# Kernel tuning notes

Hardware: AMD Instinct MI355X
Metric: run time of the kernel (lower is better)

## Reference

```python
import jax, jax.numpy as jnp
import numpy as np

B, LQ, LKV, D = 16, 2048, 2048, 64
MASK_VALUE = -1000000.0


def setup_inputs() -> dict:
    key = jax.random.key(0)
    kq, kk, kv, kl = jax.random.split(key, 4)
    queries = jax.random.normal(kq, (B, LQ, D), dtype=jnp.float32)
    keys = jax.random.normal(kk, (B, LKV, D), dtype=jnp.float32)
    values = jax.random.normal(kv, (B, LKV, D), dtype=jnp.float32)
    valid_lens = jax.random.randint(kl, (B,), 1, LKV + 1, dtype=jnp.int32)
    return {"queries": queries, "keys": keys, "values": values, "valid_lens": valid_lens}


def reference(queries, keys, values, valid_lens):
    d = queries.shape[-1]
    # scores: [B, Lq, Lkv]
    scores = jnp.einsum('bqd,bkd->bqk', queries, keys) / jnp.sqrt(jnp.float32(d))
    # valid_lens is per-batch; positions >= valid_len are masked to -1e6 (not -inf),
    # matching torch masked_fill semantics before softmax.
    col = jnp.arange(scores.shape[-1], dtype=jnp.int32)            # [Lkv]
    mask = col[None, None, :] >= valid_lens[:, None, None]          # [B, 1, Lkv] -> broadcast over Lq
    scores = jnp.where(mask, jnp.float32(MASK_VALUE), scores)
    attn = jax.nn.softmax(scores, axis=-1)
    # dropout p=0.0 (eval) -> identity
    return jnp.einsum('bqk,bkd->bqd', attn, values)
```

## Files before the change

kernel.cpp:

```cpp
#include <hip/hip_runtime.h>
#include <hip/hip_bf16.h>


#define NB   16
#define LQS  2048
#define LKVS 2048
#define DH   64
#define QBLK 64
#define KVB  64

typedef short bf16x8 __attribute__((ext_vector_type(8)));
typedef float f32x4  __attribute__((ext_vector_type(4)));

__device__ __forceinline__ unsigned short f2bf(float x) {
    return __builtin_bit_cast(unsigned short, __float2bfloat16(x));
}
__device__ __forceinline__ float bf2f(unsigned short h) {
    return __uint_as_float(((unsigned int)h) << 16);
}

__global__ __launch_bounds__(512, 4) void attn_fa(
    const float* __restrict__ Qg, const float* __restrict__ Kg,
    const float* __restrict__ Vg, const int* __restrict__ vlg,
    float* __restrict__ Og)
{
    __shared__ __align__(16) unsigned short sMem[2][4 * KVB * DH];

    const int b    = blockIdx.y;
    const int q0   = blockIdx.x * QBLK;
    const int tid  = threadIdx.x;
    const int wg   = tid >> 8;
    const int gtid = tid & 255;
    const int w4   = (tid >> 6) & 3;
    const int lane = tid & 63;
    const int lr   = lane & 15;
    const int lg   = lane >> 4;
    const int n_valid = vlg[b];

    unsigned short* sKhi = &sMem[wg][0];
    unsigned short* sKlo = &sMem[wg][4096];
    unsigned short* sVhi = &sMem[wg][8192];
    unsigned short* sVlo = &sMem[wg][12288];

    bf16x8 qhi[2], qlo[2];
    {
        const float* qp = Qg + ((size_t)b * LQS + q0 + w4 * 16 + lr) * DH;
        #pragma unroll
        for (int s = 0; s < 2; ++s) {
            const float4 a = *(const float4*)(qp + s * 32 + lg * 8);
            const float4 c = *(const float4*)(qp + s * 32 + lg * 8 + 4);
            const float vv[8] = {a.x, a.y, a.z, a.w, c.x, c.y, c.z, c.w};
            #pragma unroll
            for (int i = 0; i < 8; ++i) {
                const float x = vv[i] * 0.125f;
                const unsigned short h = f2bf(x);
                qhi[s][i] = (short)h;
                qlo[s][i] = (short)f2bf(x - bf2f(h));
            }
        }
    }

    f32x4 o[4];
    #pragma unroll
    for (int nt = 0; nt < 4; ++nt) { o[nt][0]=0.f; o[nt][1]=0.f; o[nt][2]=0.f; o[nt][3]=0.f; }
    float m_q = -__builtin_inff();
    float l_q = 0.f;

    const int nsteps = (n_valid + KVB - 1) / KVB;
    const int rounds = (nsteps + 1) >> 1;
    for (int jt = 0; jt < rounds; ++jt) {
        const int st  = 2 * jt + wg;
        const bool act = (st < nsteps);
        const int kv0 = st * KVB;
        __syncthreads();
        if (act) {
            const float* kp = Kg + ((size_t)b * LKVS + kv0) * DH;
            const float* vp = Vg + ((size_t)b * LKVS + kv0) * DH;
            #pragma unroll
            for (int it = 0; it < 4; ++it) {
                const int idx = gtid + it * 256;
                const int key = idx >> 4, f4 = idx & 15;
                const float4 kq = *(const float4*)(kp + key * DH + f4 * 4);
                const float ka[4] = {kq.x, kq.y, kq.z, kq.w};
                unsigned short kh[4], kl[4];
                #pragma unroll
                for (int i = 0; i < 4; ++i) {
                    kh[i] = f2bf(ka[i]);
                    kl[i] = f2bf(ka[i] - bf2f(kh[i]));
                }
                const int kb_ = key * 64 + (((f4 * 4) & ~7) ^ ((key & 7) << 3)) + (f4 & 1) * 4;
                *(ushort4*)(&sKhi[kb_]) = make_ushort4(kh[0], kh[1], kh[2], kh[3]);
                *(ushort4*)(&sKlo[kb_]) = make_ushort4(kl[0], kl[1], kl[2], kl[3]);
            }
            {
                const int kb = (gtid >> 4) * 4;
                const int db = (gtid & 15) * 4;
                const int pb = (kb & ~31) | (((kb >> 2) & 3) << 3) | (((kb >> 4) & 1) << 2);
                const float4 vr0 = *(const float4*)(vp + (kb + 0) * DH + db);
                const float4 vr1 = *(const float4*)(vp + (kb + 1) * DH + db);
                const float4 vr2 = *(const float4*)(vp + (kb + 2) * DH + db);
                const float4 vr3 = *(const float4*)(vp + (kb + 3) * DH + db);
                #pragma unroll
                for (int i = 0; i < 4; ++i) {
                    const int d = db + i;
                    const float f0 = (&vr0.x)[i], f1 = (&vr1.x)[i];
                    const float f2_ = (&vr2.x)[i], f3 = (&vr3.x)[i];
                    const unsigned short h0 = f2bf(f0), h1 = f2bf(f1);
                    const unsigned short h2 = f2bf(f2_), h3 = f2bf(f3);
                    const int vi = d * 64 + (pb ^ ((d & 7) << 3));
                    *(ushort4*)(&sVhi[vi]) = make_ushort4(h0, h1, h2, h3);
                    *(ushort4*)(&sVlo[vi]) = make_ushort4(
                        f2bf(f0 - bf2f(h0)), f2bf(f1 - bf2f(h1)),
                        f2bf(f2_ - bf2f(h2)), f2bf(f3 - bf2f(h3)));
                }
            }
        }
        __syncthreads();
        if (act) {
            float p_[4][4];
            __builtin_amdgcn_s_setprio(1);
            #pragma unroll
            for (int kt = 0; kt < 4; ++kt) {
                f32x4 acc = {0.f, 0.f, 0.f, 0.f};
                const int key = kt * 16 + lr;
                #pragma unroll
                for (int s = 0; s < 2; ++s) {
                    const int ki = key * 64 + ((s * 32 + lg * 8) ^ ((key & 7) << 3));
                    const bf16x8 khi = *(const bf16x8*)(&sKhi[ki]);
                    const bf16x8 klo = *(const bf16x8*)(&sKlo[ki]);
                    acc = __builtin_amdgcn_mfma_f32_16x16x32_bf16(khi, qhi[s], acc, 0, 0, 0);
                    acc = __builtin_amdgcn_mfma_f32_16x16x32_bf16(khi, qlo[s], acc, 0, 0, 0);
                    acc = __builtin_amdgcn_mfma_f32_16x16x32_bf16(klo, qhi[s], acc, 0, 0, 0);
                }
                #pragma unroll
                for (int r = 0; r < 4; ++r) p_[kt][r] = acc[r];
            }
            __builtin_amdgcn_s_setprio(0);

            if (kv0 + KVB > n_valid) {
                #pragma unroll
                for (int kt = 0; kt < 4; ++kt) {
                    #pragma unroll
                    for (int r = 0; r < 4; ++r) {
                        if (kv0 + kt * 16 + lg * 4 + r >= n_valid) p_[kt][r] = -1000000.0f;
                    }
                }
            }

            float tm = p_[0][0];
            #pragma unroll
            for (int kt = 0; kt < 4; ++kt) {
                #pragma unroll
                for (int r = 0; r < 4; ++r) tm = fmaxf(tm, p_[kt][r]);
            }
            tm = fmaxf(tm, __shfl_xor(tm, 16));
            tm = fmaxf(tm, __shfl_xor(tm, 32));
            const float mn = fmaxf(m_q, tm);
            const float sc = __expf(m_q - mn);
            float rs = 0.f;
            #pragma unroll
            for (int kt = 0; kt < 4; ++kt) {
                #pragma unroll
                for (int r = 0; r < 4; ++r) {
                    p_[kt][r] = __expf(p_[kt][r] - mn);
                    rs += p_[kt][r];
                }
            }
            rs += __shfl_xor(rs, 16);
            rs += __shfl_xor(rs, 32);
            l_q = l_q * sc + rs;
            m_q = mn;
            #pragma unroll
            for (int r = 0; r < 4; ++r) {
                const float scr = __shfl(sc, lg * 4 + r);
                #pragma unroll
                for (int nt = 0; nt < 4; ++nt) o[nt][r] *= scr;
            }

            #pragma unroll
            for (int s = 0; s < 2; ++s) {
                bf16x8 phi, plo;
                #pragma unroll
                for (int i = 0; i < 8; ++i) {
                    const float v = p_[2 * s + (i >> 2)][i & 3];
                    const unsigned short h = f2bf(v);
                    phi[i] = (short)h;
                    plo[i] = (short)f2bf(v - bf2f(h));
                }
                const int cb = s * 32 + lg * 8;
                __builtin_amdgcn_s_setprio(1);
                #pragma unroll
                for (int nt = 0; nt < 4; ++nt) {
                    const int d  = nt * 16 + lr;
                    const int vi = d * 64 + (cb ^ ((d & 7) << 3));
                    const bf16x8 vhi = *(const bf16x8*)(&sVhi[vi]);
                    const bf16x8 vlo = *(const bf16x8*)(&sVlo[vi]);
                    o[nt] = __builtin_amdgcn_mfma_f32_16x16x32_bf16(phi, vhi, o[nt], 0, 0, 0);
                    o[nt] = __builtin_amdgcn_mfma_f32_16x16x32_bf16(plo, vhi, o[nt], 0, 0, 0);
                    o[nt] = __builtin_amdgcn_mfma_f32_16x16x32_bf16(phi, vlo, o[nt], 0, 0, 0);
                }
                __builtin_amdgcn_s_setprio(0);
            }
        }
    }

    __syncthreads();
    float* fo = (float*)&sMem[0][0];
    if (wg == 1) {
        #pragma unroll
        for (int nt = 0; nt < 4; ++nt) {
            #pragma unroll
            for (int r = 0; r < 4; ++r)
                fo[(nt * 4 + r) * 256 + w4 * 64 + lane] = o[nt][r];
        }
        if (lg == 0) {
            fo[4096 + w4 * 16 + lr] = m_q;
            fo[4160 + w4 * 16 + lr] = l_q;
        }
    }
    __syncthreads();
    if (wg == 0) {
        const float m1 = fo[4096 + w4 * 16 + lr];
        const float l1 = fo[4160 + w4 * 16 + lr];
        const float mm = fmaxf(m_q, m1);
        const float a0 = __expf(m_q - mm);
        const float a1 = __expf(m1 - mm);
        const float inv = 1.0f / (a0 * l_q + a1 * l1);
        #pragma unroll
        for (int r = 0; r < 4; ++r) {
            const float a0r  = __shfl(a0, lg * 4 + r);
            const float a1r  = __shfl(a1, lg * 4 + r);
            const float invr = __shfl(inv, lg * 4 + r);
            const int row = lg * 4 + r;
            float* op = Og + ((size_t)b * LQS + q0 + w4 * 16 + row) * DH + lr;
            #pragma unroll
            for (int nt = 0; nt < 4; ++nt) {
                const float o1 = fo[(nt * 4 + r) * 256 + w4 * 64 + lane];
                op[nt * 16] = (a0r * o[nt][r] + a1r * o1) * invr;
            }
        }
    }
}

extern "C" void kernel_launch(void* const* d_in, const int* in_sizes, int n_in,
                              void* d_out, int out_size, void* d_ws, size_t ws_size,
                              hipStream_t stream) {
    (void)in_sizes; (void)n_in; (void)out_size; (void)d_ws; (void)ws_size;
    const float* Q  = (const float*)d_in[0];
    const float* K  = (const float*)d_in[1];
    const float* V  = (const float*)d_in[2];
    const int*   vl = (const int*)d_in[3];
    float* O = (float*)d_out;
    dim3 grid(LQS / QBLK, NB);
    attn_fa<<<grid, 512, 0, stream>>>(Q, K, V, vl, O);
}
```

Before: 129.3 us.

## Prefetch next K/V tile into registers during compute and change V swizzle

```diff
diff --git a/kernel.cpp b/kernel.cpp
--- a/kernel.cpp
+++ b/kernel.cpp
@@ -17,6 +17,9 @@
 }
 __device__ __forceinline__ float bf2f(unsigned short h) {
     return __uint_as_float(((unsigned int)h) << 16);
+}
+__device__ __forceinline__ int vswz(int d) {
+    return (((d & 7) ^ (d >> 3)) << 3);
 }
 
 __global__ __launch_bounds__(512, 4) void attn_fa(
@@ -42,6 +45,10 @@
     unsigned short* sVhi = &sMem[wg][8192];
     unsigned short* sVlo = &sMem[wg][12288];
 
+    const int kb = (gtid >> 4) * 4;
+    const int db = (gtid & 15) * 4;
+    const int pb = (kb & ~31) | (((kb >> 2) & 3) << 3) | (((kb >> 4) & 1) << 2);
+
     bf16x8 qhi[2], qlo[2];
     {
         const float* qp = Qg + ((size_t)b * LQS + q0 + w4 * 16 + lr) * DH;
@@ -68,20 +75,32 @@
 
     const int nsteps = (n_valid + KVB - 1) / KVB;
     const int rounds = (nsteps + 1) >> 1;
+
+    float4 kq[4], vr[4];
+    if (wg < nsteps) {
+        const float* kp = Kg + ((size_t)b * LKVS + wg * KVB) * DH;
+        const float* vp = Vg + ((size_t)b * LKVS + wg * KVB) * DH;
+        #pragma unroll
+        for (int it = 0; it < 4; ++it) {
+            const int idx = gtid + it * 256;
+            kq[it] = *(const float4*)(kp + (idx >> 4) * DH + (idx & 15) * 4);
+        }
+        #pragma unroll
+        for (int j = 0; j < 4; ++j)
+            vr[j] = *(const float4*)(vp + (kb + j) * DH + db);
+    }
+
     for (int jt = 0; jt < rounds; ++jt) {
         const int st  = 2 * jt + wg;
         const bool act = (st < nsteps);
         const int kv0 = st * KVB;
         __syncthreads();
         if (act) {
-            const float* kp = Kg + ((size_t)b * LKVS + kv0) * DH;
-            const float* vp = Vg + ((size_t)b * LKVS + kv0) * DH;
             #pragma unroll
             for (int it = 0; it < 4; ++it) {
                 const int idx = gtid + it * 256;
                 const int key = idx >> 4, f4 = idx & 15;
-                const float4 kq = *(const float4*)(kp + key * DH + f4 * 4);
-                const float ka[4] = {kq.x, kq.y, kq.z, kq.w};
+                const float ka[4] = {kq[it].x, kq[it].y, kq[it].z, kq[it].w};
                 unsigned short kh[4], kl[4];
                 #pragma unroll
                 for (int i = 0; i < 4; ++i) {
@@ -92,30 +111,38 @@
                 *(ushort4*)(&sKhi[kb_]) = make_ushort4(kh[0], kh[1], kh[2], kh[3]);
                 *(ushort4*)(&sKlo[kb_]) = make_ushort4(kl[0], kl[1], kl[2], kl[3]);
             }
-            {
-                const int kb = (gtid >> 4) * 4;
-                const int db = (gtid & 15) * 4;
-                const int pb = (kb & ~31) | (((kb >> 2) & 3) << 3) | (((kb >> 4) & 1) << 2);
-                const float4 vr0 = *(const float4*)(vp + (kb + 0) * DH + db);
-                const float4 vr1 = *(const float4*)(vp + (kb + 1) * DH + db);
-                const float4 vr2 = *(const float4*)(vp + (kb + 2) * DH + db);
-                const float4 vr3 = *(const float4*)(vp + (kb + 3) * DH + db);
-                #pragma unroll
-                for (int i = 0; i < 4; ++i) {
-                    const int d = db + i;
-                    const float f0 = (&vr0.x)[i], f1 = (&vr1.x)[i];
-                    const float f2_ = (&vr2.x)[i], f3 = (&vr3.x)[i];
-                    const unsigned short h0 = f2bf(f0), h1 = f2bf(f1);
-                    const unsigned short h2 = f2bf(f2_), h3 = f2bf(f3);
-                    const int vi = d * 64 + (pb ^ ((d & 7) << 3));
-                    *(ushort4*)(&sVhi[vi]) = make_ushort4(h0, h1, h2, h3);
-                    *(ushort4*)(&sVlo[vi]) = make_ushort4(
-                        f2bf(f0 - bf2f(h0)), f2bf(f1 - bf2f(h1)),
-                        f2bf(f2_ - bf2f(h2)), f2bf(f3 - bf2f(h3)));
-                }
+            #pragma unroll
+            for (int i = 0; i < 4; ++i) {
+                const int d = db + i;
+                const float f0 = (&vr[0].x)[i], f1 = (&vr[1].x)[i];
+                const float f2_ = (&vr[2].x)[i], f3 = (&vr[3].x)[i];
+                const unsigned short h0 = f2bf(f0), h1 = f2bf(f1);
+                const unsigned short h2 = f2bf(f2_), h3 = f2bf(f3);
+                const int vi = d * 64 + (pb ^ vswz(d));
+                *(ushort4*)(&sVhi[vi]) = make_ushort4(h0, h1, h2, h3);
+                *(ushort4*)(&sVlo[vi]) = make_ushort4(
+                    f2bf(f0 - bf2f(h0)), f2bf(f1 - bf2f(h1)),
+                    f2bf(f2_ - bf2f(h2)), f2bf(f3 - bf2f(h3)));
             }
         }
         __syncthreads();
+
+        {
+            const int stn = st + 2;
+            if (stn < nsteps) {
+                const float* kp = Kg + ((size_t)b * LKVS + stn * KVB) * DH;
+                const float* vp = Vg + ((size_t)b * LKVS + stn * KVB) * DH;
+                #pragma unroll
+                for (int it = 0; it < 4; ++it) {
+                    const int idx = gtid + it * 256;
+                    kq[it] = *(const float4*)(kp + (idx >> 4) * DH + (idx & 15) * 4);
+                }
+                #pragma unroll
+                for (int j = 0; j < 4; ++j)
+                    vr[j] = *(const float4*)(vp + (kb + j) * DH + db);
+            }
+        }
+
         if (act) {
             float p_[4][4];
             __builtin_amdgcn_s_setprio(1);
@@ -192,7 +219,7 @@
                 #pragma unroll
                 for (int nt = 0; nt < 4; ++nt) {
                     const int d  = nt * 16 + lr;
-                    const int vi = d * 64 + (cb ^ ((d & 7) << 3));
+                    const int vi = d * 64 + (cb ^ vswz(d));
                     const bf16x8 vhi = *(const bf16x8*)(&sVhi[vi]);
                     const bf16x8 vlo = *(const bf16x8*)(&sVlo[vi]);
                     o[nt] = __builtin_amdgcn_mfma_f32_16x16x32_bf16(phi, vhi, o[nt], 0, 0, 0);
```

New measurement: 119.6 us. 7.5% less time.
